# Kernel optimization log

Hardware: AMD Instinct MI355X
Metric: run time of the kernel (lower is better)

## Reference

```python
import jax, jax.numpy as jnp
import numpy as np

MEM_DIM = 2048
BATCH = 4096


def setup_inputs() -> dict:
    key = jax.random.key(0)
    ks = jax.random.split(key, 8)
    D = MEM_DIM
    scale = 1.0 / np.sqrt(D)  # torch nn.Linear default init range ~ U(-1/sqrt(D), 1/sqrt(D))
    lc = jax.random.normal(ks[0], (BATCH, D), dtype=jnp.float32)
    lh = jax.random.normal(ks[1], (BATCH, D), dtype=jnp.float32)
    rc = jax.random.normal(ks[2], (BATCH, D), dtype=jnp.float32)
    rh = jax.random.normal(ks[3], (BATCH, D), dtype=jnp.float32)
    # Fused params: columns [0:D]=input gate, [D:2D]=left forget, [2D:3D]=right forget, [3D:4D]=update
    Wl = jax.random.uniform(ks[4], (D, 4 * D), dtype=jnp.float32, minval=-scale, maxval=scale)
    Wr = jax.random.uniform(ks[5], (D, 4 * D), dtype=jnp.float32, minval=-scale, maxval=scale)
    bl = jax.random.uniform(ks[6], (4 * D,), dtype=jnp.float32, minval=-scale, maxval=scale)
    br = jax.random.uniform(ks[7], (4 * D,), dtype=jnp.float32, minval=-scale, maxval=scale)
    return {"lc": lc, "lh": lh, "rc": rc, "rh": rh, "Wl": Wl, "bl": bl, "Wr": Wr, "br": br}


def reference(lc, lh, rc, rh, Wl, bl, Wr, br):
    D = lh.shape[-1]
    # Two fused GEMMs replace 8 separate mem_dim x mem_dim linears (same math).
    g = jnp.dot(lh, Wl) + bl + jnp.dot(rh, Wr) + br  # [B, 4D]
    i = jax.nn.sigmoid(g[:, 0 * D:1 * D])   # input gate
    lf = jax.nn.sigmoid(g[:, 1 * D:2 * D])  # left forget gate
    rf = jax.nn.sigmoid(g[:, 2 * D:3 * D])  # right forget gate
    u = jnp.tanh(g[:, 3 * D:4 * D])         # cell update
    c = i * u + lf * lc + rf * rc
    h = jnp.tanh(c)
    return (c, h)
```

## Files before the change

kernel.cpp:

```cpp
#include <hip/hip_runtime.h>
#include <stdint.h>

#define D_MEM 2048
#define BATCH 4096
#define K_DIM 4096
#define N_DIM 8192

typedef __bf16 bf16x8 __attribute__((ext_vector_type(8)));
typedef float f32x4 __attribute__((ext_vector_type(4)));

typedef const void __attribute__((address_space(1)))* gas_t;
typedef void __attribute__((address_space(3)))* las_t;

__device__ __forceinline__ ushort f2b(float f) {
  union { float f; uint32_t u; } v; v.f = f;
  uint32_t u = v.u + 0x7fffu + ((v.u >> 16) & 1u);
  return (ushort)(u >> 16);
}
__device__ __forceinline__ float b2f(ushort s) {
  union { uint32_t u; float f; } v; v.u = ((uint32_t)s) << 16;
  return v.f;
}
__device__ __forceinline__ float sigm(float x) {
  return 1.0f / (1.0f + __expf(-x));
}

__global__ void cast_concat_kernel(const float* __restrict__ lh,
                                   const float* __restrict__ rh,
                                   ushort* __restrict__ A) {
  int i4 = blockIdx.x * 256 + threadIdx.x;
  int row = i4 >> 10;
  int col = (i4 & 1023) * 4;
  const float* src = (col < D_MEM) ? (lh + (size_t)row * D_MEM + col)
                                   : (rh + (size_t)row * D_MEM + (col - D_MEM));
  float4 v = *(const float4*)src;
  ushort4 o; o.x = f2b(v.x); o.y = f2b(v.y); o.z = f2b(v.z); o.w = f2b(v.w);
  *(ushort4*)(A + (size_t)row * K_DIM + col) = o;
}

__global__ void transpose_cast_kernel(const float* __restrict__ Wl,
                                      const float* __restrict__ Wr,
                                      ushort* __restrict__ Bt) {
  __shared__ float t[64 * 65];
  const float* W = blockIdx.z ? Wr : Wl;
  int n0 = blockIdx.x * 64;
  int k0 = blockIdx.y * 64;
  int tid = threadIdx.x;
#pragma unroll
  for (int i = 0; i < 4; ++i) {
    int idx = i * 256 + tid;
    int rr = idx >> 4;
    int c4 = (idx & 15) * 4;
    float4 v = *(const float4*)(W + (size_t)(k0 + rr) * N_DIM + n0 + c4);
    t[rr * 65 + c4 + 0] = v.x;
    t[rr * 65 + c4 + 1] = v.y;
    t[rr * 65 + c4 + 2] = v.z;
    t[rr * 65 + c4 + 3] = v.w;
  }
  __syncthreads();
  int kbase = (blockIdx.z ? D_MEM : 0) + k0;
#pragma unroll
  for (int i = 0; i < 4; ++i) {
    int idx = i * 256 + tid;
    int rr = idx >> 4;
    int c4 = (idx & 15) * 4;
    ushort4 o;
    o.x = f2b(t[(c4 + 0) * 65 + rr]);
    o.y = f2b(t[(c4 + 1) * 65 + rr]);
    o.z = f2b(t[(c4 + 2) * 65 + rr]);
    o.w = f2b(t[(c4 + 3) * 65 + rr]);
    *(ushort4*)(Bt + (size_t)(n0 + rr) * K_DIM + kbase + c4) = o;
  }
}

__global__ __launch_bounds__(256) void gemm_bf16_kernel(
    const ushort* __restrict__ A,
    const ushort* __restrict__ B,
    ushort* __restrict__ C) {
  const int N = N_DIM, K = K_DIM;
  __shared__ ushort As[128 * 64];
  __shared__ ushort Bs[128 * 64];
  int tid = threadIdx.x;
  int lane = tid & 63;
  int wave = tid >> 6;
  int wm = wave >> 1, wn = wave & 1;
  int q = lane >> 4, r = lane & 15;
  int m0 = blockIdx.y * 128, n0 = blockIdx.x * 128;

  int c_chunk = (tid & 7) ^ ((tid >> 3) & 7);
  int srow = tid >> 3;
  const ushort* pA = A + (size_t)(m0 + srow) * K + c_chunk * 8;
  const ushort* pB = B + (size_t)(n0 + srow) * K + c_chunk * 8;

  int aoff[4], boff[4];
#pragma unroll
  for (int f = 0; f < 4; ++f) {
    int ml = wm * 64 + f * 16 + r;
    aoff[f] = (ml * 8 + (q ^ (ml & 7))) * 16;
    int nl = wn * 64 + f * 16 + r;
    boff[f] = (nl * 8 + (q ^ (nl & 7))) * 16;
  }

  f32x4 acc[4][4];
#pragma unroll
  for (int i = 0; i < 4; ++i)
#pragma unroll
    for (int j = 0; j < 4; ++j) acc[i][j] = f32x4{0.f, 0.f, 0.f, 0.f};

  char* AsB = (char*)As;
  char* BsB = (char*)Bs;
  int ldsbase = wave * 1024;

  for (int kt = 0; kt < K / 64; ++kt) {
#pragma unroll
    for (int t2 = 0; t2 < 4; ++t2)
      __builtin_amdgcn_global_load_lds((gas_t)(pA + (size_t)t2 * 32 * K),
                                       (las_t)(AsB + t2 * 4096 + ldsbase),
                                       16, 0, 0);
#pragma unroll
    for (int t2 = 0; t2 < 4; ++t2)
      __builtin_amdgcn_global_load_lds((gas_t)(pB + (size_t)t2 * 32 * K),
                                       (las_t)(BsB + t2 * 4096 + ldsbase),
                                       16, 0, 0);
    __syncthreads();
#pragma unroll
    for (int ks = 0; ks < 2; ++ks) {
      bf16x8 af[4], bg[4];
#pragma unroll
      for (int f = 0; f < 4; ++f) {
        af[f] = *(const bf16x8*)(AsB + (aoff[f] ^ (ks * 64)));
        bg[f] = *(const bf16x8*)(BsB + (boff[f] ^ (ks * 64)));
      }
#pragma unroll
      for (int i = 0; i < 4; ++i)
#pragma unroll
        for (int j = 0; j < 4; ++j)
          acc[i][j] = __builtin_amdgcn_mfma_f32_16x16x32_bf16(
              af[i], bg[j], acc[i][j], 0, 0, 0);
    }
    __syncthreads();
    pA += 64;
    pB += 64;
  }

#pragma unroll
  for (int i = 0; i < 4; ++i) {
    int gm_base = m0 + wm * 64 + i * 16 + q * 4;
#pragma unroll
    for (int j = 0; j < 4; ++j) {
      int gn = n0 + wn * 64 + j * 16 + r;
      size_t base = (size_t)gm_base * N + gn;
#pragma unroll
      for (int e = 0; e < 4; ++e)
        C[base + (size_t)e * N] = f2b(acc[i][j][e]);
    }
  }
}

__global__ void gate_kernel(const ushort* __restrict__ G,
                            const float* __restrict__ bl,
                            const float* __restrict__ br,
                            const float* __restrict__ lc,
                            const float* __restrict__ rc,
                            float* __restrict__ out) {
  int i4 = blockIdx.x * 256 + threadIdx.x;
  int row = i4 >> 9;
  int col = (i4 & 511) * 4;
  size_t gbase = (size_t)row * N_DIM + col;

  ushort4 ui = *(const ushort4*)(G + gbase);
  ushort4 uf = *(const ushort4*)(G + gbase + 1 * D_MEM);
  ushort4 ug = *(const ushort4*)(G + gbase + 2 * D_MEM);
  ushort4 uu = *(const ushort4*)(G + gbase + 3 * D_MEM);

  float4 bli = *(const float4*)(bl + col);
  float4 blf = *(const float4*)(bl + col + 1 * D_MEM);
  float4 blr = *(const float4*)(bl + col + 2 * D_MEM);
  float4 blu = *(const float4*)(bl + col + 3 * D_MEM);
  float4 bri = *(const float4*)(br + col);
  float4 brf = *(const float4*)(br + col + 1 * D_MEM);
  float4 brr = *(const float4*)(br + col + 2 * D_MEM);
  float4 bru = *(const float4*)(br + col + 3 * D_MEM);

  float4 vlc = *(const float4*)(lc + (size_t)row * D_MEM + col);
  float4 vrc = *(const float4*)(rc + (size_t)row * D_MEM + col);

  float4 vc, vh;
  {
    float gi = b2f(ui.x) + bli.x + bri.x;
    float gf = b2f(uf.x) + blf.x + brf.x;
    float gr = b2f(ug.x) + blr.x + brr.x;
    float gu = b2f(uu.x) + blu.x + bru.x;
    vc.x = sigm(gi) * tanhf(gu) + sigm(gf) * vlc.x + sigm(gr) * vrc.x;
    vh.x = tanhf(vc.x);
  }
  {
    float gi = b2f(ui.y) + bli.y + bri.y;
    float gf = b2f(uf.y) + blf.y + brf.y;
    float gr = b2f(ug.y) + blr.y + brr.y;
    float gu = b2f(uu.y) + blu.y + bru.y;
    vc.y = sigm(gi) * tanhf(gu) + sigm(gf) * vlc.y + sigm(gr) * vrc.y;
    vh.y = tanhf(vc.y);
  }
  {
    float gi = b2f(ui.z) + bli.z + bri.z;
    float gf = b2f(uf.z) + blf.z + brf.z;
    float gr = b2f(ug.z) + blr.z + brr.z;
    float gu = b2f(uu.z) + blu.z + bru.z;
    vc.z = sigm(gi) * tanhf(gu) + sigm(gf) * vlc.z + sigm(gr) * vrc.z;
    vh.z = tanhf(vc.z);
  }
  {
    float gi = b2f(ui.w) + bli.w + bri.w;
    float gf = b2f(uf.w) + blf.w + brf.w;
    float gr = b2f(ug.w) + blr.w + brr.w;
    float gu = b2f(uu.w) + blu.w + bru.w;
    vc.w = sigm(gi) * tanhf(gu) + sigm(gf) * vlc.w + sigm(gr) * vrc.w;
    vh.w = tanhf(vc.w);
  }

  size_t obase = (size_t)row * D_MEM + col;
  *(float4*)(out + obase) = vc;
  *(float4*)(out + (size_t)BATCH * D_MEM + obase) = vh;
}

extern "C" void kernel_launch(void* const* d_in, const int* in_sizes, int n_in,
                              void* d_out, int out_size, void* d_ws, size_t ws_size,
                              hipStream_t stream) {
  const float* lc = (const float*)d_in[0];
  const float* lh = (const float*)d_in[1];
  const float* rc = (const float*)d_in[2];
  const float* rh = (const float*)d_in[3];
  const float* Wl = (const float*)d_in[4];
  const float* bl = (const float*)d_in[5];
  const float* Wr = (const float*)d_in[6];
  const float* br = (const float*)d_in[7];
  float* out = (float*)d_out;

  char* ws = (char*)d_ws;
  ushort* A  = (ushort*)ws;
  ushort* Bt = (ushort*)(ws + (size_t)32 * 1024 * 1024);
  ushort* G  = (ushort*)(ws + (size_t)96 * 1024 * 1024);

  cast_concat_kernel<<<16384, 256, 0, stream>>>(lh, rh, A);
  dim3 tg(128, 32, 2);
  transpose_cast_kernel<<<tg, 256, 0, stream>>>(Wl, Wr, Bt);
  dim3 gg(64, 32);
  gemm_bf16_kernel<<<gg, 256, 0, stream>>>(A, Bt, G);
  gate_kernel<<<8192, 256, 0, stream>>>(G, bl, br, lc, rc, out);
}
```

Baseline: 546.5 us.

## Rewrite GEMM as 256x256 tile with multi-stage LDS pipeline and fast tanh

The bf16 GEMM moves to 256x256 tiles with 512 threads, keeps 128KB of LDS as a multi-buffered ring of half-K slices, and interleaves global-to-LDS prefetch with MFMA phases using explicit barriers, waitcnt and setprio. Block indices are swizzled so neighbouring blocks share tiles in L2. The gate kernel swaps tanhf for a sigmoid-based tanh. The aim is higher MFMA utilisation by hiding load latency and reusing more data per tile. The trade-offs are heavy register pressure from 128 accumulators, a grid of 512 blocks, and slightly different numerics from the fast tanh.

```diff
diff --git a/kernel.cpp b/kernel.cpp
--- a/kernel.cpp
+++ b/kernel.cpp
@@ -23,6 +23,9 @@
 }
 __device__ __forceinline__ float sigm(float x) {
   return 1.0f / (1.0f + __expf(-x));
+}
+__device__ __forceinline__ float tanh_fast(float x) {
+  return __builtin_fmaf(2.0f, sigm(2.0f * x), -1.0f);
 }
 
 __global__ void cast_concat_kernel(const float* __restrict__ lh,
@@ -73,79 +76,115 @@
   }
 }
 
-__global__ __launch_bounds__(256) void gemm_bf16_kernel(
+__device__ __forceinline__ void stage2(const ushort* g0, const ushort* g1,
+                                       char* dst, int wave) {
+  __builtin_amdgcn_global_load_lds((gas_t)g0, (las_t)(dst + wave * 1024), 16, 0, 0);
+  __builtin_amdgcn_global_load_lds((gas_t)g1, (las_t)(dst + 8192 + wave * 1024), 16, 0, 0);
+}
+
+#define PHASE(MH, KS, BUF, G0, G1, LDST, DOVM)                                 \
+  do {                                                                         \
+    bf16x8 af[4];                                                              \
+    {                                                                          \
+      const char* ab_ = AsB + (BUF)*32768 + (KS)*16384;                        \
+      _Pragma("unroll") for (int f_ = 0; f_ < 4; ++f_)                         \
+          af[f_] = *(const bf16x8*)(ab_ + aoff[MH][f_]);                       \
+      if ((MH) == 0) {                                                         \
+        const char* bb_ = BsB + (BUF)*32768 + (KS)*16384;                      \
+        _Pragma("unroll") for (int j_ = 0; j_ < 4; ++j_)                       \
+            bfr[j_] = *(const bf16x8*)(bb_ + boff[j_]);                        \
+      }                                                                        \
+    }                                                                          \
+    stage2((G0), (G1), (LDST), wave);                                          \
+    __builtin_amdgcn_s_barrier();                                              \
+    asm volatile("s_waitcnt lgkmcnt(0)" ::: "memory");                         \
+    __builtin_amdgcn_sched_barrier(0);                                         \
+    __builtin_amdgcn_s_setprio(1);                                             \
+    _Pragma("unroll") for (int i_ = 0; i_ < 4; ++i_)                           \
+        _Pragma("unroll") for (int j_ = 0; j_ < 4; ++j_)                       \
+            acc[(MH)*4 + i_][j_] = __builtin_amdgcn_mfma_f32_16x16x32_bf16(    \
+                af[i_], bfr[j_], acc[(MH)*4 + i_][j_], 0, 0, 0);               \
+    __builtin_amdgcn_s_setprio(0);                                             \
+    if (DOVM) asm volatile("s_waitcnt vmcnt(8)" ::: "memory");                 \
+    __builtin_amdgcn_s_barrier();                                              \
+  } while (0)
+
+__global__ __launch_bounds__(512, 2) void gemm_bf16_kernel(
     const ushort* __restrict__ A,
     const ushort* __restrict__ B,
     ushort* __restrict__ C) {
-  const int N = N_DIM, K = K_DIM;
-  __shared__ ushort As[128 * 64];
-  __shared__ ushort Bs[128 * 64];
+  __shared__ char smem[131072];
+  char* AsB = smem;
+  char* BsB = smem + 65536;
+  const int K = K_DIM, N = N_DIM;
+
   int tid = threadIdx.x;
-  int lane = tid & 63;
-  int wave = tid >> 6;
-  int wm = wave >> 1, wn = wave & 1;
+  int lane = tid & 63, wave = tid >> 6;
+  int wm = wave >> 2, wn = wave & 3;
   int q = lane >> 4, r = lane & 15;
-  int m0 = blockIdx.y * 128, n0 = blockIdx.x * 128;
-
-  int c_chunk = (tid & 7) ^ ((tid >> 3) & 7);
-  int srow = tid >> 3;
-  const ushort* pA = A + (size_t)(m0 + srow) * K + c_chunk * 8;
-  const ushort* pB = B + (size_t)(n0 + srow) * K + c_chunk * 8;
-
-  int aoff[4], boff[4];
-#pragma unroll
-  for (int f = 0; f < 4; ++f) {
-    int ml = wm * 64 + f * 16 + r;
-    aoff[f] = (ml * 8 + (q ^ (ml & 7))) * 16;
-    int nl = wn * 64 + f * 16 + r;
-    boff[f] = (nl * 8 + (q ^ (nl & 7))) * 16;
-  }
-
-  f32x4 acc[4][4];
-#pragma unroll
-  for (int i = 0; i < 4; ++i)
+
+  int bid = blockIdx.x;
+  int swz = (bid & 7) * 64 + (bid >> 3);
+  int m0 = (swz >> 5) * 256;
+  int n0 = (swz & 31) * 256;
+
+  int ci0 = tid, ci1 = 512 + tid;
+  int r0 = ci0 >> 2, c0 = (ci0 & 3) ^ ((r0 ^ (r0 >> 2)) & 3);
+  int r1 = ci1 >> 2, c1 = (ci1 & 3) ^ ((r1 ^ (r1 >> 2)) & 3);
+  const ushort* sA0 = A + (size_t)(m0 + r0) * K + c0 * 8;
+  const ushort* sA1 = A + (size_t)(m0 + r1) * K + c1 * 8;
+  const ushort* sB0 = B + (size_t)(n0 + r0) * K + c0 * 8;
+  const ushort* sB1 = B + (size_t)(n0 + r1) * K + c1 * 8;
+
+  int swzr = (r ^ (r >> 2)) & 3;
+  int aoff[2][4], boff[4];
+#pragma unroll
+  for (int mh = 0; mh < 2; ++mh)
+#pragma unroll
+    for (int f = 0; f < 4; ++f) {
+      int row = wm * 128 + mh * 64 + f * 16 + r;
+      aoff[mh][f] = row * 64 + (q ^ swzr) * 16;
+    }
+#pragma unroll
+  for (int j = 0; j < 4; ++j) {
+    int col = wn * 64 + j * 16 + r;
+    boff[j] = col * 64 + (q ^ swzr) * 16;
+  }
+
+  f32x4 acc[8][4];
+#pragma unroll
+  for (int i = 0; i < 8; ++i)
 #pragma unroll
     for (int j = 0; j < 4; ++j) acc[i][j] = f32x4{0.f, 0.f, 0.f, 0.f};
-
-  char* AsB = (char*)As;
-  char* BsB = (char*)Bs;
-  int ldsbase = wave * 1024;
-
-  for (int kt = 0; kt < K / 64; ++kt) {
-#pragma unroll
-    for (int t2 = 0; t2 < 4; ++t2)
-      __builtin_amdgcn_global_load_lds((gas_t)(pA + (size_t)t2 * 32 * K),
-                                       (las_t)(AsB + t2 * 4096 + ldsbase),
-                                       16, 0, 0);
-#pragma unroll
-    for (int t2 = 0; t2 < 4; ++t2)
-      __builtin_amdgcn_global_load_lds((gas_t)(pB + (size_t)t2 * 32 * K),
-                                       (las_t)(BsB + t2 * 4096 + ldsbase),
-                                       16, 0, 0);
-    __syncthreads();
-#pragma unroll
-    for (int ks = 0; ks < 2; ++ks) {
-      bf16x8 af[4], bg[4];
-#pragma unroll
-      for (int f = 0; f < 4; ++f) {
-        af[f] = *(const bf16x8*)(AsB + (aoff[f] ^ (ks * 64)));
-        bg[f] = *(const bf16x8*)(BsB + (boff[f] ^ (ks * 64)));
-      }
-#pragma unroll
-      for (int i = 0; i < 4; ++i)
-#pragma unroll
-        for (int j = 0; j < 4; ++j)
-          acc[i][j] = __builtin_amdgcn_mfma_f32_16x16x32_bf16(
-              af[i], bg[j], acc[i][j], 0, 0, 0);
-    }
-    __syncthreads();
-    pA += 64;
-    pB += 64;
-  }
-
-#pragma unroll
-  for (int i = 0; i < 4; ++i) {
-    int gm_base = m0 + wm * 64 + i * 16 + q * 4;
+  bf16x8 bfr[4];
+
+  stage2(sA0,      sA1,      AsB + 0,     wave);
+  stage2(sB0,      sB1,      BsB + 0,     wave);
+  stage2(sA0 + 32, sA1 + 32, AsB + 16384, wave);
+  stage2(sB0 + 32, sB1 + 32, BsB + 16384, wave);
+  stage2(sA0 + 64, sA1 + 64, AsB + 32768, wave);
+  stage2(sB0 + 64, sB1 + 64, BsB + 32768, wave);
+  asm volatile("s_waitcnt vmcnt(8)" ::: "memory");
+  __builtin_amdgcn_s_barrier();
+
+#pragma unroll 1
+  for (int t = 0; t < 64; t += 2) {
+    const int o1 = (t + 1) * 64;
+    const int o2 = (t + 2 < 64 ? t + 2 : 63) * 64;
+    const int o3 = (t + 3 < 64 ? t + 3 : 63) * 64;
+    PHASE(0, 0, 0, sA0 + o1 + 32, sA1 + o1 + 32, AsB + 49152, 0);
+    PHASE(1, 0, 0, sB0 + o1 + 32, sB1 + o1 + 32, BsB + 49152, 1);
+    PHASE(0, 1, 0, sA0 + o2,      sA1 + o2,      AsB + 0,     0);
+    PHASE(1, 1, 0, sB0 + o2,      sB1 + o2,      BsB + 0,     1);
+    PHASE(0, 0, 1, sA0 + o2 + 32, sA1 + o2 + 32, AsB + 16384, 0);
+    PHASE(1, 0, 1, sB0 + o2 + 32, sB1 + o2 + 32, BsB + 16384, 1);
+    PHASE(0, 1, 1, sA0 + o3,      sA1 + o3,      AsB + 32768, 0);
+    PHASE(1, 1, 1, sB0 + o3,      sB1 + o3,      BsB + 32768, 1);
+  }
+
+#pragma unroll
+  for (int i = 0; i < 8; ++i) {
+    int gm_base = m0 + wm * 128 + i * 16 + q * 4;
 #pragma unroll
     for (int j = 0; j < 4; ++j) {
       int gn = n0 + wn * 64 + j * 16 + r;
@@ -191,32 +230,32 @@
     float gf = b2f(uf.x) + blf.x + brf.x;
     float gr = b2f(ug.x) + blr.x + brr.x;
     float gu = b2f(uu.x) + blu.x + bru.x;
-    vc.x = sigm(gi) * tanhf(gu) + sigm(gf) * vlc.x + sigm(gr) * vrc.x;
-    vh.x = tanhf(vc.x);
+    vc.x = sigm(gi) * tanh_fast(gu) + sigm(gf) * vlc.x + sigm(gr) * vrc.x;
+    vh.x = tanh_fast(vc.x);
   }
   {
     float gi = b2f(ui.y) + bli.y + bri.y;
     float gf = b2f(uf.y) + blf.y + brf.y;
     float gr = b2f(ug.y) + blr.y + brr.y;
     float gu = b2f(uu.y) + blu.y + bru.y;
-    vc.y = sigm(gi) * tanhf(gu) + sigm(gf) * vlc.y + sigm(gr) * vrc.y;
-    vh.y = tanhf(vc.y);
+    vc.y = sigm(gi) * tanh_fast(gu) + sigm(gf) * vlc.y + sigm(gr) * vrc.y;
+    vh.y = tanh_fast(vc.y);
   }
   {
     float gi = b2f(ui.z) + bli.z + bri.z;
     float gf = b2f(uf.z) + blf.z + brf.z;
     float gr = b2f(ug.z) + blr.z + brr.z;
     float gu = b2f(uu.z) + blu.z + bru.z;
-    vc.z = sigm(gi) * tanhf(gu) + sigm(gf) * vlc.z + sigm(gr) * vrc.z;
-    vh.z = tanhf(vc.z);
+    vc.z = sigm(gi) * tanh_fast(gu) + sigm(gf) * vlc.z + sigm(gr) * vrc.z;
+    vh.z = tanh_fast(vc.z);
   }
   {
     float gi = b2f(ui.w) + bli.w + bri.w;
     float gf = b2f(uf.w) + blf.w + brf.w;
     float gr = b2f(ug.w) + blr.w + brr.w;
     float gu = b2f(uu.w) + blu.w + bru.w;
-    vc.w = sigm(gi) * tanhf(gu) + sigm(gf) * vlc.w + sigm(gr) * vrc.w;
-    vh.w = tanhf(vc.w);
+    vc.w = sigm(gi) * tanh_fast(gu) + sigm(gf) * vlc.w + sigm(gr) * vrc.w;
+    vh.w = tanh_fast(vc.w);
   }
 
   size_t obase = (size_t)row * D_MEM + col;
@@ -245,7 +284,6 @@
   cast_concat_kernel<<<16384, 256, 0, stream>>>(lh, rh, A);
   dim3 tg(128, 32, 2);
   transpose_cast_kernel<<<tg, 256, 0, stream>>>(Wl, Wr, Bt);
-  dim3 gg(64, 32);
-  gemm_bf16_kernel<<<gg, 256, 0, stream>>>(A, Bt, G);
+  gemm_bf16_kernel<<<512, 512, 0, stream>>>(A, Bt, G);
   gate_kernel<<<8192, 256, 0, stream>>>(G, bl, br, lc, rc, out);
 }
```

Result: no change. 546.6 us (+0.0%).
